# Optimization experiments

Hardware: AMD Instinct MI355X
Metric: run time of the kernel (lower is better)

Reference implementation:

```python
import jax, jax.numpy as jnp
import numpy as np

B, F, V, E, A = 8192, 39, 1_000_000, 16, 16  # batch, fields, vocab, embed, attn


def setup_inputs() -> dict:
    key = jax.random.key(0)
    ks = jax.random.split(key, 9)
    return {
        "feat_index": jax.random.randint(ks[0], (B, F), 0, V),
        "feat_value": jax.random.uniform(ks[1], (B, F), dtype=jnp.float32),
        "first_order_weights": jax.random.normal(ks[2], (V, 1), dtype=jnp.float32) * 0.01,
        "emb_table": jax.random.normal(ks[3], (V, E), dtype=jnp.float32) * 0.01,
        "bias": jax.random.normal(ks[4], (1,), dtype=jnp.float32),
        "attention_w": jax.random.normal(ks[5], (E, A), dtype=jnp.float32) * 0.1,
        "attention_b": jax.random.normal(ks[6], (A,), dtype=jnp.float32) * 0.1,
        "projection_h": jax.random.normal(ks[7], (A, 1), dtype=jnp.float32) * 0.1,
        "projection_p": jax.random.normal(ks[8], (E, 1), dtype=jnp.float32) * 0.1,
    }


def reference(feat_index, feat_value, first_order_weights, emb_table, bias,
              attention_w, attention_b, projection_h, projection_p):
    fv = feat_value[..., None]                                  # [B,F,1]
    # first order: gather weights, scale by value, sum over fields
    y_first = jnp.sum(first_order_weights[feat_index] * fv, axis=1)[:, 0]  # [B]
    # embeddings scaled by feature values
    emb = emb_table[feat_index] * fv                            # [B,F,E]
    # pairwise bi-interaction over all i<j field pairs (num_pairs = F*(F-1)/2)
    iu, ju = np.triu_indices(F, k=1)
    bi = emb[:, iu, :] * emb[:, ju, :]                          # [B,P,E]
    # tiny attention MLP + softmax over pairs
    att = jax.nn.relu(jnp.einsum('bpe,ea->bpa', bi, attention_w) + attention_b)
    score = jax.nn.softmax(jnp.einsum('bpa,ao->bpo', att, projection_h), axis=1)  # [B,P,1]
    pooled = jnp.sum(score * bi, axis=1)                        # [B,E]
    aw = (pooled @ projection_p)[:, 0]                          # [B]
    y = bias + y_first + aw                                     # [B]
    return jax.nn.sigmoid(y)
```

## Files before the change

kernel.cpp:

```cpp
#include <hip/hip_runtime.h>
#include <hip/hip_fp16.h>
#include <math.h>


#define BB 8192
#define FF 39
#define PP 741
#define NT 24
#define RBYTES 48
#define SBYTES (FF * RBYTES)

typedef _Float16 f16x8 __attribute__((ext_vector_type(8)));
typedef _Float16 h2    __attribute__((ext_vector_type(2)));
typedef __fp16   hw2   __attribute__((ext_vector_type(2)));
typedef float    f32x4  __attribute__((ext_vector_type(4)));
typedef float    f32x16 __attribute__((ext_vector_type(16)));

struct alignas(16) PijT { unsigned v[32][NT]; };
static constexpr PijT make_pij() {
    PijT t{};
    int p = 0;
    for (int i = 0; i < FF; ++i)
        for (int j = i + 1; j < FF; ++j) {
            t.v[p & 31][p >> 5] =
                ((unsigned)(i * RBYTES) << 16) | (unsigned)(j * RBYTES);
            ++p;
        }
    return t;
}
__device__ constexpr PijT c_pij = make_pij();

static __device__ __forceinline__ h2 cvt2(float lo, float hi) {
    return __builtin_bit_cast(h2, __builtin_amdgcn_cvt_pkrtz(lo, hi));
}
static __device__ __forceinline__ h2 ash2(unsigned d) {
    return __builtin_bit_cast(h2, d);
}
static __device__ __forceinline__ float fdot2f(h2 a, h2 b, float c) {
    return __builtin_amdgcn_fdot2(__builtin_bit_cast(hw2, a),
                                  __builtin_bit_cast(hw2, b), c, false);
}
static __device__ __forceinline__ h2 relu2(h2 x) {
    const h2 zz = {(_Float16)0.f, (_Float16)0.f};
    return __builtin_elementwise_max(x, zz);
}

__global__ __launch_bounds__(256, 5)
void afm_kernel(const int*   __restrict__ fidx,
                const float* __restrict__ fval,
                const float* __restrict__ fow,
                const float* __restrict__ emb,
                const float* __restrict__ bias,
                const float* __restrict__ aw_,
                const float* __restrict__ ab_,
                const float* __restrict__ ph_,
                const float* __restrict__ pp_,
                float*       __restrict__ out)
{
    __shared__ __align__(16) unsigned char s_emb[4 * SBYTES];

    const int tid  = threadIdx.x;
    const int wid  = tid >> 6;
    const int lane = tid & 63;
    const int n    = lane & 31;
    const int h    = lane >> 5;
    const int smp  = blockIdx.x * 4 + wid;

    int ixr = 0; float vr = 0.f;
    if (lane < FF) {
        ixr = fidx[smp * FF + lane];
        vr  = fval[smp * FF + lane];
    }

    unsigned char* my = s_emb + wid * SBYTES;
    for (int u = lane; u < FF * 2; u += 64) {
        int row = u >> 1, hh = u & 1;
        int   ix = __shfl(ixr, row);
        float v  = __shfl(vr,  row);
        const float4* src = (const float4*)emb + (size_t)ix * 4 + hh * 2;
        float4 e0 = src[0], e1 = src[1];
        h2 a0 = cvt2(e0.x * v, e0.y * v);
        h2 a1 = cvt2(e0.z * v, e0.w * v);
        h2 a2 = cvt2(e1.x * v, e1.y * v);
        h2 a3 = cvt2(e1.z * v, e1.w * v);
        uint4 d = make_uint4(__builtin_bit_cast(unsigned, a0),
                             __builtin_bit_cast(unsigned, a1),
                             __builtin_bit_cast(unsigned, a2),
                             __builtin_bit_cast(unsigned, a3));
        *(uint4*)(my + row * RBYTES + hh * 16) = d;
    }

    float fo = (lane < FF) ? fow[ixr] * vr : 0.f;

    const float LOG2E = 1.44269504088896f;
    h2 hp0, hp1, hp2, hp3;
    {
        const f32x4 lo = ((const f32x4*)ph_)[h];
        const f32x4 hi = ((const f32x4*)ph_)[h + 2];
        hp0 = cvt2(lo[0] * LOG2E, lo[1] * LOG2E);
        hp1 = cvt2(lo[2] * LOG2E, lo[3] * LOG2E);
        hp2 = cvt2(hi[0] * LOG2E, hi[1] * LOG2E);
        hp3 = cvt2(hi[2] * LOG2E, hi[3] * LOG2E);
    }

    f32x16 cinit;
    {
        const f32x4 ab_lo = ((const f32x4*)ab_)[h];
        const f32x4 ab_hi = ((const f32x4*)ab_)[h + 2];
        cinit[0] = ab_lo[0]; cinit[1] = ab_lo[1];
        cinit[2] = ab_lo[2]; cinit[3] = ab_lo[3];
        cinit[4] = ab_hi[0]; cinit[5] = ab_hi[1];
        cinit[6] = ab_hi[2]; cinit[7] = ab_hi[3];
        #pragma unroll
        for (int r = 8; r < 16; ++r) cinit[r] = 0.f;
    }

    f16x8 wfrag;
    {
        float t0 = 0.f, t1 = 0.f, t2 = 0.f, t3 = 0.f,
              t4 = 0.f, t5 = 0.f, t6 = 0.f, t7 = 0.f;
        if (n < 16) {
            const float* base = aw_ + (8 * h) * 16 + n;
            t0 = base[0];   t1 = base[16];  t2 = base[32];  t3 = base[48];
            t4 = base[64];  t5 = base[80];  t6 = base[96];  t7 = base[112];
        } else if (n == 16) {
            const float* base = pp_ + 8 * h;
            t0 = base[0]; t1 = base[1]; t2 = base[2]; t3 = base[3];
            t4 = base[4]; t5 = base[5]; t6 = base[6]; t7 = base[7];
        }
        union { h2 hh[4]; f16x8 v; } u;
        u.hh[0] = cvt2(t0, t1); u.hh[1] = cvt2(t2, t3);
        u.hh[2] = cvt2(t4, t5); u.hh[3] = cvt2(t6, t7);
        wfrag = u.v;
    }

    unsigned po[NT];
    {
        const uint4* myp4 = (const uint4*)c_pij.v[n];
        #pragma unroll
        for (int g = 0; g < 6; ++g) {
            uint4 q = myp4[g];
            po[4 * g + 0] = q.x; po[4 * g + 1] = q.y;
            po[4 * g + 2] = q.z; po[4 * g + 3] = q.w;
        }
    }

    const unsigned char* bpre = my + h * 16;
    float aw = 0.f;
    float z  = 0.f;

    uint4 di = *(const uint4*)(bpre + (po[0] >> 16));
    uint4 dj = *(const uint4*)(bpre + (po[0] & 0xFFFFu));

    #pragma unroll
    for (int t = 0; t < NT; ++t) {
        uint4 diN = di, djN = dj;
        if (t + 1 < NT) {
            diN = *(const uint4*)(bpre + (po[t + 1] >> 16));
            djN = *(const uint4*)(bpre + (po[t + 1] & 0xFFFFu));
        }
        h2 m0 = ash2(di.x) * ash2(dj.x);
        h2 m1 = ash2(di.y) * ash2(dj.y);
        h2 m2 = ash2(di.z) * ash2(dj.z);
        h2 m3 = ash2(di.w) * ash2(dj.w);
        union { h2 hh[4]; f16x8 v; } u;
        u.hh[0] = m0; u.hh[1] = m1; u.hh[2] = m2; u.hh[3] = m3;
        f32x16 d = __builtin_amdgcn_mfma_f32_32x32x16_f16(wfrag, u.v,
                                                          cinit, 0, 0, 0);
        h2 c0 = relu2(cvt2(d[0], d[1]));
        h2 c1 = relu2(cvt2(d[2], d[3]));
        h2 c2 = relu2(cvt2(d[4], d[5]));
        h2 c3 = relu2(cvt2(d[6], d[7]));
        float s = fdot2f(c0, hp0,
                  fdot2f(c1, hp1,
                  fdot2f(c2, hp2,
                  fdot2f(c3, hp3, 0.f))));
        s += __shfl_xor(s, 32);
        float w = __builtin_amdgcn_exp2f(s);
        if (t == NT - 1) w = (n < PP - (NT - 1) * 32) ? w : 0.f;
        z  += w;
        aw  = fmaf(w, d[8], aw);
        di = diN; dj = djN;
    }

    #pragma unroll
    for (int m = 1; m < 64; m <<= 1) {
        aw += __shfl_xor(aw, m);
        z  += __shfl_xor(z, m);
        fo += __shfl_xor(fo, m);
    }
    if (lane == 0) {
        float y = bias[0] + fo + 2.f * aw / z;
        out[smp] = 1.f / (1.f + __expf(-y));
    }
}

extern "C" void kernel_launch(void* const* d_in, const int* in_sizes, int n_in,
                              void* d_out, int out_size, void* d_ws, size_t ws_size,
                              hipStream_t stream) {
    const int*   fidx      = (const int*)  d_in[0];
    const float* fval      = (const float*)d_in[1];
    const float* fow       = (const float*)d_in[2];
    const float* emb_table = (const float*)d_in[3];
    const float* bias      = (const float*)d_in[4];
    const float* attn_w    = (const float*)d_in[5];
    const float* attn_b    = (const float*)d_in[6];
    const float* proj_h    = (const float*)d_in[7];
    const float* proj_p    = (const float*)d_in[8];
    float* out = (float*)d_out;

    afm_kernel<<<BB / 4, 256, 0, stream>>>(fidx, fval, fow, emb_table, bias,
                                           attn_w, attn_b, proj_h, proj_p, out);
}
```

Measured before the change: 123.9 us.

## Process two samples per wave and prefetch the second sample's embeddings during compute

Each wavefront now handles two batch samples. It issues the global embedding gathers for the second sample before running the MFMA pair loop on the first, then packs and stores them into LDS afterwards. The goal is to hide gather latency behind compute and to amortise the weight, fragment and offset-table setup over two samples. The cost is more registers, with launch bounds lowered from 5 to 4 blocks per SM, twice the LDS per block, and half as many blocks in the grid.

```diff
diff --git a/kernel.cpp b/kernel.cpp
--- a/kernel.cpp
+++ b/kernel.cpp
@@ -44,114 +44,24 @@
     const h2 zz = {(_Float16)0.f, (_Float16)0.f};
     return __builtin_elementwise_max(x, zz);
 }
-
-__global__ __launch_bounds__(256, 5)
-void afm_kernel(const int*   __restrict__ fidx,
-                const float* __restrict__ fval,
-                const float* __restrict__ fow,
-                const float* __restrict__ emb,
-                const float* __restrict__ bias,
-                const float* __restrict__ aw_,
-                const float* __restrict__ ab_,
-                const float* __restrict__ ph_,
-                const float* __restrict__ pp_,
-                float*       __restrict__ out)
+static __device__ __forceinline__ uint4 packrow(float4 e0, float4 e1, float v) {
+    h2 a0 = cvt2(e0.x * v, e0.y * v);
+    h2 a1 = cvt2(e0.z * v, e0.w * v);
+    h2 a2 = cvt2(e1.x * v, e1.y * v);
+    h2 a3 = cvt2(e1.z * v, e1.w * v);
+    return make_uint4(__builtin_bit_cast(unsigned, a0),
+                      __builtin_bit_cast(unsigned, a1),
+                      __builtin_bit_cast(unsigned, a2),
+                      __builtin_bit_cast(unsigned, a3));
+}
+
+static __device__ __forceinline__ void tile_loop(
+    const unsigned char* bpre, const unsigned* po, f16x8 wfrag,
+    const f32x16& cinit, h2 hp0, h2 hp1, h2 hp2, h2 hp3, int n,
+    float& aw, float& z)
 {
-    __shared__ __align__(16) unsigned char s_emb[4 * SBYTES];
-
-    const int tid  = threadIdx.x;
-    const int wid  = tid >> 6;
-    const int lane = tid & 63;
-    const int n    = lane & 31;
-    const int h    = lane >> 5;
-    const int smp  = blockIdx.x * 4 + wid;
-
-    int ixr = 0; float vr = 0.f;
-    if (lane < FF) {
-        ixr = fidx[smp * FF + lane];
-        vr  = fval[smp * FF + lane];
-    }
-
-    unsigned char* my = s_emb + wid * SBYTES;
-    for (int u = lane; u < FF * 2; u += 64) {
-        int row = u >> 1, hh = u & 1;
-        int   ix = __shfl(ixr, row);
-        float v  = __shfl(vr,  row);
-        const float4* src = (const float4*)emb + (size_t)ix * 4 + hh * 2;
-        float4 e0 = src[0], e1 = src[1];
-        h2 a0 = cvt2(e0.x * v, e0.y * v);
-        h2 a1 = cvt2(e0.z * v, e0.w * v);
-        h2 a2 = cvt2(e1.x * v, e1.y * v);
-        h2 a3 = cvt2(e1.z * v, e1.w * v);
-        uint4 d = make_uint4(__builtin_bit_cast(unsigned, a0),
-                             __builtin_bit_cast(unsigned, a1),
-                             __builtin_bit_cast(unsigned, a2),
-                             __builtin_bit_cast(unsigned, a3));
-        *(uint4*)(my + row * RBYTES + hh * 16) = d;
-    }
-
-    float fo = (lane < FF) ? fow[ixr] * vr : 0.f;
-
-    const float LOG2E = 1.44269504088896f;
-    h2 hp0, hp1, hp2, hp3;
-    {
-        const f32x4 lo = ((const f32x4*)ph_)[h];
-        const f32x4 hi = ((const f32x4*)ph_)[h + 2];
-        hp0 = cvt2(lo[0] * LOG2E, lo[1] * LOG2E);
-        hp1 = cvt2(lo[2] * LOG2E, lo[3] * LOG2E);
-        hp2 = cvt2(hi[0] * LOG2E, hi[1] * LOG2E);
-        hp3 = cvt2(hi[2] * LOG2E, hi[3] * LOG2E);
-    }
-
-    f32x16 cinit;
-    {
-        const f32x4 ab_lo = ((const f32x4*)ab_)[h];
-        const f32x4 ab_hi = ((const f32x4*)ab_)[h + 2];
-        cinit[0] = ab_lo[0]; cinit[1] = ab_lo[1];
-        cinit[2] = ab_lo[2]; cinit[3] = ab_lo[3];
-        cinit[4] = ab_hi[0]; cinit[5] = ab_hi[1];
-        cinit[6] = ab_hi[2]; cinit[7] = ab_hi[3];
-        #pragma unroll
-        for (int r = 8; r < 16; ++r) cinit[r] = 0.f;
-    }
-
-    f16x8 wfrag;
-    {
-        float t0 = 0.f, t1 = 0.f, t2 = 0.f, t3 = 0.f,
-              t4 = 0.f, t5 = 0.f, t6 = 0.f, t7 = 0.f;
-        if (n < 16) {
-            const float* base = aw_ + (8 * h) * 16 + n;
-            t0 = base[0];   t1 = base[16];  t2 = base[32];  t3 = base[48];
-            t4 = base[64];  t5 = base[80];  t6 = base[96];  t7 = base[112];
-        } else if (n == 16) {
-            const float* base = pp_ + 8 * h;
-            t0 = base[0]; t1 = base[1]; t2 = base[2]; t3 = base[3];
-            t4 = base[4]; t5 = base[5]; t6 = base[6]; t7 = base[7];
-        }
-        union { h2 hh[4]; f16x8 v; } u;
-        u.hh[0] = cvt2(t0, t1); u.hh[1] = cvt2(t2, t3);
-        u.hh[2] = cvt2(t4, t5); u.hh[3] = cvt2(t6, t7);
-        wfrag = u.v;
-    }
-
-    unsigned po[NT];
-    {
-        const uint4* myp4 = (const uint4*)c_pij.v[n];
-        #pragma unroll
-        for (int g = 0; g < 6; ++g) {
-            uint4 q = myp4[g];
-            po[4 * g + 0] = q.x; po[4 * g + 1] = q.y;
-            po[4 * g + 2] = q.z; po[4 * g + 3] = q.w;
-        }
-    }
-
-    const unsigned char* bpre = my + h * 16;
-    float aw = 0.f;
-    float z  = 0.f;
-
     uint4 di = *(const uint4*)(bpre + (po[0] >> 16));
     uint4 dj = *(const uint4*)(bpre + (po[0] & 0xFFFFu));
-
     #pragma unroll
     for (int t = 0; t < NT; ++t) {
         uint4 diN = di, djN = dj;
@@ -182,16 +92,142 @@
         aw  = fmaf(w, d[8], aw);
         di = diN; dj = djN;
     }
+}
+
+__global__ __launch_bounds__(256, 4)
+void afm_kernel(const int*   __restrict__ fidx,
+                const float* __restrict__ fval,
+                const float* __restrict__ fow,
+                const float* __restrict__ emb,
+                const float* __restrict__ bias,
+                const float* __restrict__ aw_,
+                const float* __restrict__ ab_,
+                const float* __restrict__ ph_,
+                const float* __restrict__ pp_,
+                float*       __restrict__ out)
+{
+    __shared__ __align__(16) unsigned char s_emb[8 * SBYTES];
+
+    const int tid  = threadIdx.x;
+    const int wid  = tid >> 6;
+    const int lane = tid & 63;
+    const int n    = lane & 31;
+    const int h    = lane >> 5;
+    const int smp0 = blockIdx.x * 8 + wid * 2;
+
+    const int rowA = lane >> 1, hhA = lane & 1;
+    const int rowB = rowA + 32, hhB = hhA;
+    const bool okB = (lane < FF * 2 - 64);
+    const int rowBc = okB ? rowB : FF - 1;
+
+    int ix0 = 0, ix1 = 0; float v0 = 0.f, v1 = 0.f;
+    if (lane < FF) {
+        ix0 = fidx[smp0 * FF + lane];       v0 = fval[smp0 * FF + lane];
+        ix1 = fidx[(smp0 + 1) * FF + lane]; v1 = fval[(smp0 + 1) * FF + lane];
+    }
+    float fo0 = (lane < FF) ? fow[ix0] * v0 : 0.f;
+    float fo1 = (lane < FF) ? fow[ix1] * v1 : 0.f;
+
+    unsigned char* my0 = s_emb + (wid * 2) * SBYTES;
+    unsigned char* my1 = my0 + SBYTES;
+
+    {
+        int   ia = __shfl(ix0, rowA); float va = __shfl(v0, rowA);
+        const float4* sa = (const float4*)emb + (size_t)ia * 4 + hhA * 2;
+        float4 e0 = sa[0], e1 = sa[1];
+        *(uint4*)(my0 + rowA * RBYTES + hhA * 16) = packrow(e0, e1, va);
+        if (okB) {
+            int   ib = __shfl(ix0, rowBc); float vb = __shfl(v0, rowBc);
+            const float4* sb = (const float4*)emb + (size_t)ib * 4 + hhB * 2;
+            float4 f0 = sb[0], f1 = sb[1];
+            *(uint4*)(my0 + rowB * RBYTES + hhB * 16) = packrow(f0, f1, vb);
+        }
+    }
+
+    float4 pA0, pA1, pB0, pB1;
+    float  vA1, vB1;
+    {
+        int ia = __shfl(ix1, rowA); vA1 = __shfl(v1, rowA);
+        const float4* sa = (const float4*)emb + (size_t)ia * 4 + hhA * 2;
+        pA0 = sa[0]; pA1 = sa[1];
+        int ib = __shfl(ix1, rowBc); vB1 = __shfl(v1, rowBc);
+        if (okB) {
+            const float4* sb = (const float4*)emb + (size_t)ib * 4 + hhB * 2;
+            pB0 = sb[0]; pB1 = sb[1];
+        }
+    }
+
+    const float LOG2E = 1.44269504088896f;
+    h2 hp0, hp1, hp2, hp3;
+    {
+        const f32x4 lo = ((const f32x4*)ph_)[h];
+        const f32x4 hi = ((const f32x4*)ph_)[h + 2];
+        hp0 = cvt2(lo[0] * LOG2E, lo[1] * LOG2E);
+        hp1 = cvt2(lo[2] * LOG2E, lo[3] * LOG2E);
+        hp2 = cvt2(hi[0] * LOG2E, hi[1] * LOG2E);
+        hp3 = cvt2(hi[2] * LOG2E, hi[3] * LOG2E);
+    }
+    f32x16 cinit;
+    {
+        const f32x4 ab_lo = ((const f32x4*)ab_)[h];
+        const f32x4 ab_hi = ((const f32x4*)ab_)[h + 2];
+        cinit[0] = ab_lo[0]; cinit[1] = ab_lo[1];
+        cinit[2] = ab_lo[2]; cinit[3] = ab_lo[3];
+        cinit[4] = ab_hi[0]; cinit[5] = ab_hi[1];
+        cinit[6] = ab_hi[2]; cinit[7] = ab_hi[3];
+        #pragma unroll
+        for (int r = 8; r < 16; ++r) cinit[r] = 0.f;
+    }
+    f16x8 wfrag;
+    {
+        float t0 = 0.f, t1 = 0.f, t2 = 0.f, t3 = 0.f,
+              t4 = 0.f, t5 = 0.f, t6 = 0.f, t7 = 0.f;
+        if (n < 16) {
+            const float* base = aw_ + (8 * h) * 16 + n;
+            t0 = base[0];   t1 = base[16];  t2 = base[32];  t3 = base[48];
+            t4 = base[64];  t5 = base[80];  t6 = base[96];  t7 = base[112];
+        } else if (n == 16) {
+            const float* base = pp_ + 8 * h;
+            t0 = base[0]; t1 = base[1]; t2 = base[2]; t3 = base[3];
+            t4 = base[4]; t5 = base[5]; t6 = base[6]; t7 = base[7];
+        }
+        union { h2 hh[4]; f16x8 v; } u;
+        u.hh[0] = cvt2(t0, t1); u.hh[1] = cvt2(t2, t3);
+        u.hh[2] = cvt2(t4, t5); u.hh[3] = cvt2(t6, t7);
+        wfrag = u.v;
+    }
+
+    unsigned po[NT];
+    {
+        const uint4* myp4 = (const uint4*)c_pij.v[n];
+        #pragma unroll
+        for (int g = 0; g < 6; ++g) {
+            uint4 q = myp4[g];
+            po[4 * g + 0] = q.x; po[4 * g + 1] = q.y;
+            po[4 * g + 2] = q.z; po[4 * g + 3] = q.w;
+        }
+    }
+
+    float aw0 = 0.f, z0 = 0.f, aw1 = 0.f, z1 = 0.f;
+    tile_loop(my0 + h * 16, po, wfrag, cinit, hp0, hp1, hp2, hp3, n, aw0, z0);
+
+    *(uint4*)(my1 + rowA * RBYTES + hhA * 16) = packrow(pA0, pA1, vA1);
+    if (okB)
+        *(uint4*)(my1 + rowB * RBYTES + hhB * 16) = packrow(pB0, pB1, vB1);
+    tile_loop(my1 + h * 16, po, wfrag, cinit, hp0, hp1, hp2, hp3, n, aw1, z1);
 
     #pragma unroll
     for (int m = 1; m < 64; m <<= 1) {
-        aw += __shfl_xor(aw, m);
-        z  += __shfl_xor(z, m);
-        fo += __shfl_xor(fo, m);
+        aw0 += __shfl_xor(aw0, m); z0 += __shfl_xor(z0, m);
+        fo0 += __shfl_xor(fo0, m);
+        aw1 += __shfl_xor(aw1, m); z1 += __shfl_xor(z1, m);
+        fo1 += __shfl_xor(fo1, m);
     }
     if (lane == 0) {
-        float y = bias[0] + fo + 2.f * aw / z;
-        out[smp] = 1.f / (1.f + __expf(-y));
+        float y0 = bias[0] + fo0 + 2.f * aw0 / z0;
+        float y1 = bias[0] + fo1 + 2.f * aw1 / z1;
+        out[smp0]     = 1.f / (1.f + __expf(-y0));
+        out[smp0 + 1] = 1.f / (1.f + __expf(-y1));
     }
 }
 
@@ -209,6 +245,6 @@
     const float* proj_p    = (const float*)d_in[8];
     float* out = (float*)d_out;
 
-    afm_kernel<<<BB / 4, 256, 0, stream>>>(fidx, fval, fow, emb_table, bias,
+    afm_kernel<<<BB / 8, 256, 0, stream>>>(fidx, fval, fow, emb_table, bias,
                                            attn_w, attn_b, proj_h, proj_p, out);
 }
```

Result: slower. 281.7 us (+127.4%).
